# Performance work log

Hardware: AMD Instinct MI355X
Metric: run time of the kernel (lower is better)

## Reference

```python
import jax, jax.numpy as jnp
import numpy as np

B, N, D, H, DH, E, BIAS_DIM = 8, 512, 512, 8, 64, 32768, 8

def setup_inputs() -> dict:
    key = jax.random.key(0)
    ks = jax.random.split(key, 10)
    states = jax.random.normal(ks[0], (B, N, D), jnp.float32)
    key_states = jax.random.normal(ks[1], (B, N, D), jnp.float32)
    # causal mask, broadcastable over heads: [B,1,N,N]
    masks = jnp.broadcast_to(jnp.tril(jnp.ones((N, N), jnp.float32)), (B, 1, N, N))
    edge_type = jax.random.randint(ks[2], (E, 1), 0, BIAS_DIM, jnp.int32)
    b_idx = jax.random.randint(ks[3], (E, 1), 0, B, jnp.int32)
    q_idx = jax.random.randint(ks[4], (E, 1), 0, N, jnp.int32)
    k_idx = jax.random.randint(ks[5], (E, 1), 0, N, jnp.int32)
    attention_bias = jnp.concatenate([edge_type, b_idx, q_idx, k_idx], axis=1)
    s = 0.05
    Wq = jax.random.normal(ks[6], (D, H, DH), jnp.float32) * s
    Wk = jax.random.normal(ks[7], (D, H, DH), jnp.float32) * s
    Wv = jax.random.normal(ks[8], (D, H, DH), jnp.float32) * s
    k2 = jax.random.split(ks[9], 3)
    Wo = jax.random.normal(k2[0], (H, DH, D), jnp.float32) * s
    bias_embs = jax.random.normal(k2[1], (BIAS_DIM, DH), jnp.float32) * s
    bias_scalar = jax.random.normal(k2[2], (DH, 1), jnp.float32) * s
    return {"states": states, "key_states": key_states, "masks": masks,
            "attention_bias": attention_bias, "Wq": Wq, "Wk": Wk, "Wv": Wv,
            "Wo": Wo, "bias_embs": bias_embs, "bias_scalar": bias_scalar}

def reference(states, key_states, masks, attention_bias, Wq, Wk, Wv, Wo, bias_embs, bias_scalar):
    q = jnp.einsum('btd,dha->btha', states, Wq)
    k = jnp.einsum('btd,dha->btha', key_states, Wk)
    v = jnp.einsum('btd,dha->btha', key_states, Wv)
    alpha = jnp.einsum('bkha,bqha->bhqk', k, q)  # [B,H,Q,K]
    # sparse edge bias: embed edge types, project to scalar, scatter into [B,Q,K]
    et = attention_bias[:, 0]
    bias_vals = (bias_embs[et] @ bias_scalar)[:, 0]  # [E]
    bq, bk = alpha.shape[2], alpha.shape[3]
    bias_mat = jnp.zeros((alpha.shape[0], bq, bk), alpha.dtype)
    bias_mat = bias_mat.at[attention_bias[:, 1], attention_bias[:, 2], attention_bias[:, 3]].add(bias_vals)
    summed_keys = jnp.sum(k, axis=-1)  # [B,K,H]
    alpha = alpha + jnp.einsum('bqk,bkh->bhqk', bias_mat, summed_keys)
    alpha = alpha * jax.lax.rsqrt(jnp.float32(DH))
    neg = jnp.finfo(jnp.float32).min
    alpha = alpha * masks + (1.0 - jnp.ceil(masks)) * neg
    alpha = jax.nn.softmax(alpha, axis=-1)
    alpha = alpha * masks
    context = jnp.einsum('bhqk,bkha->bqha', alpha, v)
    return jnp.einsum('btha,had->btd', context, Wo)
```

## Files before the change

### kernel.cpp

```cpp
#include <hip/hip_runtime.h>

typedef unsigned short u16;
typedef unsigned int u32;
typedef __bf16 bf16x8 __attribute__((ext_vector_type(8)));
typedef float f32x4 __attribute__((ext_vector_type(4)));
typedef u16 u16x8 __attribute__((ext_vector_type(8)));
typedef u16 u16x4 __attribute__((ext_vector_type(4)));


__device__ __forceinline__ u16 f2b(float f) {
  union { float f; u32 i; } v; v.f = f;
  u32 r = v.i + 0x7fffu + ((v.i >> 16) & 1u);
  return (u16)(r >> 16);
}

#define GLL16(gp, lp)                                                      \
  __builtin_amdgcn_global_load_lds(                                       \
      (const __attribute__((address_space(1))) u32*)(gp),                 \
      (__attribute__((address_space(3))) u32*)(lp), 16, 0, 0)

__device__ __forceinline__ void stage64(const u16* g, u16* l, int wave, int lane) {
  int rsub = lane >> 3;
  int gs = (((lane & 7) ^ rsub) << 3);
  #pragma unroll
  for (int c = 0; c < 2; c++) {
    int ch = wave * 2 + c;
    GLL16(g + (size_t)(ch * 8 + rsub) * 512 + gs, l + ch * 512);
  }
}
__device__ __forceinline__ void stage128(const u16* g, u16* l, int wave, int lane) {
  int rsub = lane >> 3;
  int gs = (((lane & 7) ^ rsub) << 3);
  #pragma unroll
  for (int c = 0; c < 4; c++) {
    int ch = wave * 4 + c;
    GLL16(g + (size_t)(ch * 8 + rsub) * 512 + gs, l + ch * 512);
  }
}
__device__ __forceinline__ int swz(int row, int g) {
  return row * 64 + ((g ^ (row & 7)) << 3);
}

__global__ __launch_bounds__(256) void prologue(
    const float* __restrict__ states, const float* __restrict__ key_states,
    const float* __restrict__ Wq, const float* __restrict__ Wk,
    const float* __restrict__ Wv, const float* __restrict__ Wo,
    u16* __restrict__ sb, u16* __restrict__ kbin, u16* __restrict__ wbase,
    float* __restrict__ bias_mat) {
  __shared__ u16 t[32][33];
  int bid = blockIdx.x;
  int tid = threadIdx.x;
  if (bid < 2048) {
    const float* src = (bid >= 1024) ? key_states : states;
    u16* dst = (bid >= 1024) ? kbin : sb;
    int gid = (bid & 1023) * 256 + tid;
    const float4* sp = (const float4*)src + (size_t)gid * 2;
    float4 x0 = sp[0], x1 = sp[1];
    u16x8 p;
    p[0] = f2b(x0.x); p[1] = f2b(x0.y); p[2] = f2b(x0.z); p[3] = f2b(x0.w);
    p[4] = f2b(x1.x); p[5] = f2b(x1.y); p[6] = f2b(x1.z); p[7] = f2b(x1.w);
    *(u16x8*)(dst + (size_t)gid * 8) = p;
  } else if (bid < 3072) {
    int tt = bid - 2048;
    int z = tt >> 8, rem = tt & 255;
    int bx = rem & 15, by = rem >> 4;
    const float* src; float sc = 1.f;
    if (z == 0)      { src = Wq; sc = 0.125f; }
    else if (z == 1) { src = Wk; }
    else if (z == 2) { src = Wv; }
    else             { src = Wo; }
    u16* dst = wbase + (size_t)z * 262144;
    int tx = tid & 31, ty = tid >> 5;
    int c0 = bx * 32, r0 = by * 32;
    #pragma unroll
    for (int i = ty; i < 32; i += 8) t[i][tx] = f2b(src[(r0 + i) * 512 + c0 + tx] * sc);
    __syncthreads();
    #pragma unroll
    for (int i = ty; i < 32; i += 8) dst[(c0 + i) * 512 + r0 + tx] = t[tx][i];
  } else {
    int i = (bid - 3072) * 256 + tid;
    float4 z4 = {0.f, 0.f, 0.f, 0.f};
    ((float4*)bias_mat)[i] = z4;
  }
}

__global__ __launch_bounds__(256) void qkv_gemm(const u16* __restrict__ sb,
                                                const u16* __restrict__ kbin,
                                                const u16* __restrict__ wT,
                                                const int* __restrict__ ab,
                                                const float* __restrict__ be,
                                                const float* __restrict__ bsc,
                                                float* __restrict__ bias_m,
                                                u16* __restrict__ qb,
                                                u16* __restrict__ kbo,
                                                u16* __restrict__ vtb,
                                                float* __restrict__ summed,
                                                int n_edges) {
  __shared__ alignas(16) u16 As[2][64 * 64];
  __shared__ alignas(16) u16 Bs[2][128 * 64];
  __shared__ float ssum[4][64];
  __shared__ float tvs[8];
  int tid = threadIdx.x;
  int lane = tid & 63, wave = tid >> 6;
  int quad = lane >> 4, ln = lane & 15;
  int fb = blockIdx.y * 64 + blockIdx.x;

  if (tid < 8) {
    const float4* bev = (const float4*)(be + tid * 64);
    const float4* bscv = (const float4*)bsc;
    float s = 0.f;
    #pragma unroll
    for (int a4 = 0; a4 < 16; a4++) {
      float4 x = bev[a4], y = bscv[a4];
      s += x.x * y.x + x.y * y.y + x.z * y.z + x.w * y.w;
    }
    tvs[tid] = s * 0.125f;
  }
  __syncthreads();
  for (int e = fb * 256 + tid; e < n_edges; e += 768 * 256) {
    int et = ab[e * 4 + 0];
    int b  = ab[e * 4 + 1];
    int qi = ab[e * 4 + 2];
    int ki = ab[e * 4 + 3];
    atomicAdd(&bias_m[((size_t)b * 512 + qi) * 512 + ki], tvs[et]);
  }

  int row0 = blockIdx.x * 64;
  int col0 = blockIdx.y * 128;
  const u16* A = (col0 < 512) ? sb : kbin;
  const u16* Ab = A + (size_t)row0 * 512;
  const u16* Bb = wT + (size_t)col0 * 512;

  f32x4 acc[4][2];
  #pragma unroll
  for (int i = 0; i < 4; i++)
    #pragma unroll
    for (int j = 0; j < 2; j++) acc[i][j] = (f32x4){0.f, 0.f, 0.f, 0.f};

  stage64(Ab, As[0], wave, lane);
  stage128(Bb, Bs[0], wave, lane);

  int cur = 0;
  for (int k0 = 0; k0 < 512; k0 += 64) {
    __syncthreads();
    if (k0 < 448) {
      stage64(Ab + k0 + 64, As[cur ^ 1], wave, lane);
      stage128(Bb + k0 + 64, Bs[cur ^ 1], wave, lane);
    }
    #pragma unroll
    for (int s = 0; s < 2; s++) {
      bf16x8 af[4], bfv[2];
      #pragma unroll
      for (int i = 0; i < 4; i++)
        af[i] = *(bf16x8*)&As[cur][swz(i * 16 + ln, s * 4 + quad)];
      #pragma unroll
      for (int j = 0; j < 2; j++)
        bfv[j] = *(bf16x8*)&Bs[cur][swz(wave * 32 + j * 16 + ln, s * 4 + quad)];
      #pragma unroll
      for (int i = 0; i < 4; i++)
        #pragma unroll
        for (int j = 0; j < 2; j++)
          acc[i][j] = __builtin_amdgcn_mfma_f32_16x16x32_bf16(af[i], bfv[j], acc[i][j], 0, 0, 0);
    }
    cur ^= 1;
  }

  int region = col0 >> 9;
  int nbase = col0 & 511;
  if (region <= 1) {
    u16* Cout = region ? kbo : qb;
    #pragma unroll
    for (int i = 0; i < 4; i++)
      #pragma unroll
      for (int j = 0; j < 2; j++) {
        int mb = row0 + i * 16 + quad * 4;
        int n = nbase + wave * 32 + j * 16 + ln;
        #pragma unroll
        for (int r = 0; r < 4; r++)
          Cout[(size_t)(mb + r) * 512 + n] = f2b(acc[i][j][r]);
      }
    if (region == 1) {
      #pragma unroll
      for (int i = 0; i < 4; i++)
        #pragma unroll
        for (int r = 0; r < 4; r++) {
          float v = acc[i][0][r] + acc[i][1][r];
          v += __shfl_xor(v, 1);
          v += __shfl_xor(v, 2);
          v += __shfl_xor(v, 4);
          v += __shfl_xor(v, 8);
          if (ln == 0) ssum[wave][i * 16 + quad * 4 + r] = v;
        }
      __syncthreads();
      if (tid < 128) {
        int hl = tid >> 6, row = tid & 63;
        float s = ssum[hl * 2][row] + ssum[hl * 2 + 1][row];
        int m = row0 + row;
        int b = m >> 9, t = m & 511;
        int h = (nbase >> 6) + hl;
        summed[((size_t)(b * 8 + h)) * 512 + t] = s;
      }
    }
  } else {
    #pragma unroll
    for (int i = 0; i < 4; i++)
      #pragma unroll
      for (int j = 0; j < 2; j++) {
        int mb = row0 + i * 16 + quad * 4;
        int bb = mb >> 9, t0 = mb & 511;
        int a_abs = nbase + wave * 32 + j * 16 + ln;
        int h = a_abs >> 6, a = a_abs & 63;
        u16x4 p;
        p[0] = f2b(acc[i][j][0]); p[1] = f2b(acc[i][j][1]);
        p[2] = f2b(acc[i][j][2]); p[3] = f2b(acc[i][j][3]);
        *(u16x4*)&vtb[(((size_t)bb * 8 + h) * 64 + a) * 512 + t0] = p;
      }
  }
}

__global__ __launch_bounds__(256) void attn_mfma(const u16* __restrict__ q,
                                                 const u16* __restrict__ k,
                                                 const u16* __restrict__ vt,
                                                 const float* __restrict__ bias_mat,
                                                 const float* __restrict__ summed,
                                                 u16* __restrict__ ctx,
                                                 float* __restrict__ Opart,
                                                 float* __restrict__ ml) {
  __shared__ alignas(16) u16 Qs[64 * 64];
  __shared__ alignas(16) u16 Ks[2][64 * 64];
  __shared__ alignas(16) u16 Vs[2][64 * 64];
  __shared__ alignas(16) u16 Ps[4][16 * 72];
  int tid = threadIdx.x;
  int wave = tid >> 6, lane = tid & 63;
  int quad = lane >> 4, ln = lane & 15;
  int p2 = blockIdx.x;
  int bh, u;
  {
    const int fours[6] = {3, 4, 6, 8, 10, 11};
    const int threes[2] = {2, 9};
    const int ones[2] = {0, 5};
    const int twos[2] = {1, 7};
    if (p2 < 384)      { bh = p2 & 63; u = fours[p2 >> 6]; }
    else if (p2 < 512) { int q2 = p2 - 384; bh = q2 & 63; u = threes[q2 >> 6]; }
    else if (p2 < 640) { int q2 = p2 - 512; bh = q2 & 63; u = ones[q2 >> 6]; }
    else               { int q2 = p2 - 640; bh = q2 & 63; u = twos[q2 >> 6]; }
  }
  int b = bh >> 3, h = bh & 7;
  int qt, kb0, kbe, part = 0;
  bool partial;
  if (u < 4) { qt = u; kb0 = 0; kbe = u; partial = false; }
  else {
    int v = u - 4; qt = 4 + (v >> 1); part = v & 1; partial = true;
    if (part == 0) { kb0 = 0; kbe = 3; } else { kb0 = 4; kbe = qt; }
  }
  int q0 = qt * 64;

  const u16* qb_ = q + ((size_t)(b * 512 + q0)) * 512 + h * 64;
  const u16* kb_ = k + ((size_t)(b * 512)) * 512 + h * 64;
  const u16* vb_ = vt + ((size_t)bh * 64) * 512;

  stage64(qb_, Qs, wave, lane);
  stage64(kb_ + (size_t)kb0 * 64 * 512, Ks[0], wave, lane);
  stage64(vb_ + kb0 * 64, Vs[0], wave, lane);

  float m_r[4], l_r[4];
  f32x4 o[4];
  #pragma unroll
  for (int r = 0; r < 4; r++) { m_r[r] = -3.40282347e38f; l_r[r] = 0.f; }
  #pragma unroll
  for (int nt = 0; nt < 4; nt++) o[nt] = (f32x4){0.f, 0.f, 0.f, 0.f};

  int qrow = q0 + wave * 16 + quad * 4;

  float c_skv[4], c_bias[4][4];
  #pragma unroll
  for (int nt = 0; nt < 4; nt++) {
    int t = kb0 * 64 + nt * 16 + ln;
    c_skv[nt] = summed[bh * 512 + t];
    const float* bp2 = bias_mat + ((size_t)(b * 512 + qrow)) * 512 + t;
    #pragma unroll
    for (int r = 0; r < 4; r++) c_bias[nt][r] = bp2[(size_t)r * 512];
  }

  int cur = 0;
  for (int kb = kb0; kb <= kbe; kb++) {
    __syncthreads();

    float n_skv[4], n_bias[4][4];
    if (kb < kbe) {
      stage64(kb_ + (size_t)(kb + 1) * 64 * 512, Ks[cur ^ 1], wave, lane);
      stage64(vb_ + (kb + 1) * 64, Vs[cur ^ 1], wave, lane);
      #pragma unroll
      for (int nt = 0; nt < 4; nt++) {
        int t = (kb + 1) * 64 + nt * 16 + ln;
        n_skv[nt] = summed[bh * 512 + t];
        const float* bp2 = bias_mat + ((size_t)(b * 512 + qrow)) * 512 + t;
        #pragma unroll
        for (int r = 0; r < 4; r++) n_bias[nt][r] = bp2[(size_t)r * 512];
      }
    }

    bf16x8 aq0 = *(bf16x8*)&Qs[swz(wave * 16 + ln, quad)];
    bf16x8 aq1 = *(bf16x8*)&Qs[swz(wave * 16 + ln, 4 + quad)];
    f32x4 s[4];
    #pragma unroll
    for (int nt = 0; nt < 4; nt++) {
      bf16x8 b0 = *(bf16x8*)&Ks[cur][swz(nt * 16 + ln, quad)];
      bf16x8 b1 = *(bf16x8*)&Ks[cur][swz(nt * 16 + ln, 4 + quad)];
      s[nt] = (f32x4){0.f, 0.f, 0.f, 0.f};
      s[nt] = __builtin_amdgcn_mfma_f32_16x16x32_bf16(aq0, b0, s[nt], 0, 0, 0);
      s[nt] = __builtin_amdgcn_mfma_f32_16x16x32_bf16(aq1, b1, s[nt], 0, 0, 0);
    }

    #pragma unroll
    for (int nt = 0; nt < 4; nt++) {
      int t = kb * 64 + nt * 16 + ln;
      #pragma unroll
      for (int r = 0; r < 4; r++) {
        float val = s[nt][r] + c_bias[nt][r] * c_skv[nt];
        s[nt][r] = (t <= qrow + r) ? val : -3.40282347e38f;
      }
    }

    float alpha[4];
    #pragma unroll
    for (int r = 0; r < 4; r++) {
      float tm = fmaxf(fmaxf(s[0][r], s[1][r]), fmaxf(s[2][r], s[3][r]));
      #pragma unroll
      for (int off = 8; off; off >>= 1) tm = fmaxf(tm, __shfl_xor(tm, off));
      float mn = fmaxf(m_r[r], tm);
      alpha[r] = __expf(m_r[r] - mn);
      m_r[r] = mn;
      float rs = 0.f;
      #pragma unroll
      for (int nt = 0; nt < 4; nt++) {
        float pp = __expf(s[nt][r] - mn);
        s[nt][r] = pp;
        rs += pp;
      }
      #pragma unroll
      for (int off = 8; off; off >>= 1) rs += __shfl_xor(rs, off);
      l_r[r] = l_r[r] * alpha[r] + rs;
    }

    #pragma unroll
    for (int nt = 0; nt < 4; nt++)
      #pragma unroll
      for (int r = 0; r < 4; r++)
        Ps[wave][(quad * 4 + r) * 72 + nt * 16 + ln] = f2b(s[nt][r]);
    #pragma unroll
    for (int nt = 0; nt < 4; nt++)
      #pragma unroll
      for (int r = 0; r < 4; r++)
        o[nt][r] *= alpha[r];

    bf16x8 ap0 = *(bf16x8*)&Ps[wave][ln * 72 + quad * 8];
    bf16x8 ap1 = *(bf16x8*)&Ps[wave][ln * 72 + 32 + quad * 8];
    #pragma unroll
    for (int nt = 0; nt < 4; nt++) {
      bf16x8 b0 = *(bf16x8*)&Vs[cur][swz(nt * 16 + ln, quad)];
      bf16x8 b1 = *(bf16x8*)&Vs[cur][swz(nt * 16 + ln, 4 + quad)];
      o[nt] = __builtin_amdgcn_mfma_f32_16x16x32_bf16(ap0, b0, o[nt], 0, 0, 0);
      o[nt] = __builtin_amdgcn_mfma_f32_16x16x32_bf16(ap1, b1, o[nt], 0, 0, 0);
    }

    if (kb < kbe) {
      #pragma unroll
      for (int nt = 0; nt < 4; nt++) {
        c_skv[nt] = n_skv[nt];
        #pragma unroll
        for (int r = 0; r < 4; r++) c_bias[nt][r] = n_bias[nt][r];
      }
    }
    cur ^= 1;
  }

  if (!partial) {
    #pragma unroll
    for (int r = 0; r < 4; r++) {
      float inv = 1.f / l_r[r];
      int qr2 = qrow + r;
      u16* dst = ctx + ((size_t)(b * 512 + qr2)) * 512 + h * 64;
      #pragma unroll
      for (int nt = 0; nt < 4; nt++)
        dst[nt * 16 + ln] = f2b(o[nt][r] * inv);
    }
  } else {
    #pragma unroll
    for (int r = 0; r < 4; r++) {
      int row = qrow + r - 256;
      float* dst = Opart + (((size_t)(part * 64 + bh)) * 256 + row) * 64;
      #pragma unroll
      for (int nt = 0; nt < 4; nt++)
        dst[nt * 16 + ln] = o[nt][r];
    }
    if (ln == 0) {
      #pragma unroll
      for (int r = 0; r < 4; r++) {
        int row = qrow + r - 256;
        float* mp = ml + (((size_t)(part * 64 + bh)) * 256 + row) * 2;
        mp[0] = m_r[r];
        mp[1] = l_r[r];
      }
    }
  }
}

__device__ __forceinline__ void merge_stage(const float* __restrict__ Opart,
                                            const float* __restrict__ mlbuf,
                                            int row0, int k0, u16* dst, int tid) {
  int gi = tid * 2;
  int r = gi >> 3, g = gi & 7;
  int trow = (row0 & 511) - 256 + r;
  int b = row0 >> 9;
  int h = k0 >> 6;
  size_t i0 = ((size_t)(b * 8 + h)) * 256 + trow;
  size_t i1 = i0 + 64 * 256;
  float m0 = mlbuf[i0 * 2], l0 = mlbuf[i0 * 2 + 1];
  float m1 = mlbuf[i1 * 2], l1 = mlbuf[i1 * 2 + 1];
  float m = fmaxf(m0, m1);
  float a0 = __expf(m0 - m), a1 = __expf(m1 - m);
  float linv = 1.f / (l0 * a0 + l1 * a1);
  a0 *= linv; a1 *= linv;
  const float4* p0 = (const float4*)(Opart + i0 * 64 + g * 8);
  const float4* p1 = (const float4*)(Opart + i1 * 64 + g * 8);
  u16x8 q0, q1;
  #pragma unroll
  for (int c = 0; c < 2; c++) {
    float4 x0 = p0[c], x1 = p1[c];
    q0[c * 4 + 0] = f2b(x0.x * a0 + x1.x * a1);
    q0[c * 4 + 1] = f2b(x0.y * a0 + x1.y * a1);
    q0[c * 4 + 2] = f2b(x0.z * a0 + x1.z * a1);
    q0[c * 4 + 3] = f2b(x0.w * a0 + x1.w * a1);
  }
  #pragma unroll
  for (int c = 2; c < 4; c++) {
    float4 x0 = p0[c], x1 = p1[c];
    q1[(c - 2) * 4 + 0] = f2b(x0.x * a0 + x1.x * a1);
    q1[(c - 2) * 4 + 1] = f2b(x0.y * a0 + x1.y * a1);
    q1[(c - 2) * 4 + 2] = f2b(x0.z * a0 + x1.z * a1);
    q1[(c - 2) * 4 + 3] = f2b(x0.w * a0 + x1.w * a1);
  }
  *(u16x8*)&dst[swz(r, g)] = q0;
  *(u16x8*)&dst[swz(r, g + 1)] = q1;
}

__global__ __launch_bounds__(256) void out_gemm(const u16* __restrict__ A,
                                                const u16* __restrict__ BT,
                                                const float* __restrict__ Opart,
                                                const float* __restrict__ mlbuf,
                                                float* __restrict__ C) {
  __shared__ alignas(16) u16 As[2][64 * 64];
  __shared__ alignas(16) u16 Bs[2][64 * 64];
  int tid = threadIdx.x;
  int lane = tid & 63, wave = tid >> 6;
  int quad = lane >> 4, ln = lane & 15;
  int wr = wave >> 1, wc = wave & 1;
  int row0 = blockIdx.x * 64;
  int col0 = blockIdx.y * 64;
  bool mergeA = (row0 & 511) >= 256;
  const u16* Ab = A + (size_t)row0 * 512;
  const u16* Bb = BT + (size_t)col0 * 512;

  f32x4 acc[2][2];
  #pragma unroll
  for (int i = 0; i < 2; i++)
    #pragma unroll
    for (int j = 0; j < 2; j++) acc[i][j] = (f32x4){0.f, 0.f, 0.f, 0.f};

  if (mergeA) merge_stage(Opart, mlbuf, row0, 0, As[0], tid);
  else        stage64(Ab, As[0], wave, lane);
  stage64(Bb, Bs[0], wave, lane);

  int cur = 0;
  for (int k0 = 0; k0 < 512; k0 += 64) {
    __syncthreads();
    if (k0 < 448) {
      if (mergeA) merge_stage(Opart, mlbuf, row0, k0 + 64, As[cur ^ 1], tid);
      else        stage64(Ab + k0 + 64, As[cur ^ 1], wave, lane);
      stage64(Bb + k0 + 64, Bs[cur ^ 1], wave, lane);
    }
    #pragma unroll
    for (int s = 0; s < 2; s++) {
      bf16x8 af[2], bfv[2];
      #pragma unroll
      for (int i = 0; i < 2; i++)
        af[i] = *(bf16x8*)&As[cur][swz(wr * 32 + i * 16 + ln, s * 4 + quad)];
      #pragma unroll
      for (int j = 0; j < 2; j++)
        bfv[j] = *(bf16x8*)&Bs[cur][swz(wc * 32 + j * 16 + ln, s * 4 + quad)];
      #pragma unroll
      for (int i = 0; i < 2; i++)
        #pragma unroll
        for (int j = 0; j < 2; j++)
          acc[i][j] = __builtin_amdgcn_mfma_f32_16x16x32_bf16(af[i], bfv[j], acc[i][j], 0, 0, 0);
    }
    cur ^= 1;
  }
  #pragma unroll
  for (int i = 0; i < 2; i++)
    #pragma unroll
    for (int j = 0; j < 2; j++) {
      int mb = row0 + wr * 32 + i * 16 + quad * 4;
      int n = col0 + wc * 32 + j * 16 + ln;
      #pragma unroll
      for (int r = 0; r < 4; r++)
        C[(size_t)(mb + r) * 512 + n] = acc[i][j][r];
    }
}

extern "C" void kernel_launch(void* const* d_in, const int* in_sizes, int n_in,
                              void* d_out, int out_size, void* d_ws, size_t ws_size,
                              hipStream_t stream) {
  const float* states     = (const float*)d_in[0];
  const float* key_states = (const float*)d_in[1];
  const int*   ab         = (const int*)d_in[3];
  const float* Wq         = (const float*)d_in[4];
  const float* Wk         = (const float*)d_in[5];
  const float* Wv         = (const float*)d_in[6];
  const float* Wo         = (const float*)d_in[7];
  const float* be         = (const float*)d_in[8];
  const float* bsc        = (const float*)d_in[9];
  float* out = (float*)d_out;

  char* ws = (char*)d_ws;
  const size_t MB = 1024 * 1024;
  u16* wbase    = (u16*)(ws);
  u16* wot      = (u16*)(ws + 1536 * 1024);
  u16* sb       = (u16*)(ws + 2 * MB);
  u16* kbin     = (u16*)(ws + 6 * MB);
  u16* qb       = (u16*)(ws + 10 * MB);
  u16* kbo      = (u16*)(ws + 14 * MB);
  u16* vtb      = (u16*)(ws + 18 * MB);
  u16* ctxb     = (u16*)(ws + 22 * MB);
  float* bias_m = (float*)(ws + 26 * MB);
  float* summed = (float*)(ws + 34 * MB);
  float* Opart  = (float*)(ws + 35 * MB);
  float* mlbuf  = (float*)(ws + 43 * MB);

  int n_edges = in_sizes[3] / 4;

  prologue<<<dim3(5120), 256, 0, stream>>>(
      states, key_states, Wq, Wk, Wv, Wo, sb, kbin, wbase, bias_m);
  qkv_gemm<<<dim3(64, 12), 256, 0, stream>>>(
      sb, kbin, wbase, ab, be, bsc, bias_m, qb, kbo, vtb, summed, n_edges);
  attn_mfma<<<dim3(768), 256, 0, stream>>>(qb, kbo, vtb, bias_m, summed, ctxb, Opart, mlbuf);
  out_gemm<<<dim3(64, 8), 256, 0, stream>>>(ctxb, wot, Opart, mlbuf, out);
}
```

Before: 133.5 us.

## Fuse fp32-to-bf16 conversion and weight transpose into GEMM staging loops

Removes the prologue kernel that converted activations and weights to bf16 and transposed the weights into workspace. The qkv and output GEMMs now load fp32 data into registers, convert and transpose while writing to LDS, and prefetch the next tile in registers. The bias matrix is zeroed with hipMemsetAsync instead. This saves a kernel launch and a round trip of the converted data through memory. In exchange it adds an extra barrier per k-step, converts the weights redundantly in every block, and uses strided scalar weight loads in place of async global-to-LDS copies.

```diff
diff --git a/kernel.cpp b/kernel.cpp
--- a/kernel.cpp
+++ b/kernel.cpp
@@ -28,65 +28,15 @@
     GLL16(g + (size_t)(ch * 8 + rsub) * 512 + gs, l + ch * 512);
   }
 }
-__device__ __forceinline__ void stage128(const u16* g, u16* l, int wave, int lane) {
-  int rsub = lane >> 3;
-  int gs = (((lane & 7) ^ rsub) << 3);
-  #pragma unroll
-  for (int c = 0; c < 4; c++) {
-    int ch = wave * 4 + c;
-    GLL16(g + (size_t)(ch * 8 + rsub) * 512 + gs, l + ch * 512);
-  }
-}
 __device__ __forceinline__ int swz(int row, int g) {
   return row * 64 + ((g ^ (row & 7)) << 3);
 }
 
-__global__ __launch_bounds__(256) void prologue(
-    const float* __restrict__ states, const float* __restrict__ key_states,
-    const float* __restrict__ Wq, const float* __restrict__ Wk,
-    const float* __restrict__ Wv, const float* __restrict__ Wo,
-    u16* __restrict__ sb, u16* __restrict__ kbin, u16* __restrict__ wbase,
-    float* __restrict__ bias_mat) {
-  __shared__ u16 t[32][33];
-  int bid = blockIdx.x;
-  int tid = threadIdx.x;
-  if (bid < 2048) {
-    const float* src = (bid >= 1024) ? key_states : states;
-    u16* dst = (bid >= 1024) ? kbin : sb;
-    int gid = (bid & 1023) * 256 + tid;
-    const float4* sp = (const float4*)src + (size_t)gid * 2;
-    float4 x0 = sp[0], x1 = sp[1];
-    u16x8 p;
-    p[0] = f2b(x0.x); p[1] = f2b(x0.y); p[2] = f2b(x0.z); p[3] = f2b(x0.w);
-    p[4] = f2b(x1.x); p[5] = f2b(x1.y); p[6] = f2b(x1.z); p[7] = f2b(x1.w);
-    *(u16x8*)(dst + (size_t)gid * 8) = p;
-  } else if (bid < 3072) {
-    int tt = bid - 2048;
-    int z = tt >> 8, rem = tt & 255;
-    int bx = rem & 15, by = rem >> 4;
-    const float* src; float sc = 1.f;
-    if (z == 0)      { src = Wq; sc = 0.125f; }
-    else if (z == 1) { src = Wk; }
-    else if (z == 2) { src = Wv; }
-    else             { src = Wo; }
-    u16* dst = wbase + (size_t)z * 262144;
-    int tx = tid & 31, ty = tid >> 5;
-    int c0 = bx * 32, r0 = by * 32;
-    #pragma unroll
-    for (int i = ty; i < 32; i += 8) t[i][tx] = f2b(src[(r0 + i) * 512 + c0 + tx] * sc);
-    __syncthreads();
-    #pragma unroll
-    for (int i = ty; i < 32; i += 8) dst[(c0 + i) * 512 + r0 + tx] = t[tx][i];
-  } else {
-    int i = (bid - 3072) * 256 + tid;
-    float4 z4 = {0.f, 0.f, 0.f, 0.f};
-    ((float4*)bias_mat)[i] = z4;
-  }
-}
-
-__global__ __launch_bounds__(256) void qkv_gemm(const u16* __restrict__ sb,
-                                                const u16* __restrict__ kbin,
-                                                const u16* __restrict__ wT,
+__global__ __launch_bounds__(256) void qkv_gemm(const float* __restrict__ states,
+                                                const float* __restrict__ key_states,
+                                                const float* __restrict__ Wq,
+                                                const float* __restrict__ Wk,
+                                                const float* __restrict__ Wv,
                                                 const int* __restrict__ ab,
                                                 const float* __restrict__ be,
                                                 const float* __restrict__ bsc,
@@ -127,9 +77,16 @@
 
   int row0 = blockIdx.x * 64;
   int col0 = blockIdx.y * 128;
-  const u16* A = (col0 < 512) ? sb : kbin;
-  const u16* Ab = A + (size_t)row0 * 512;
-  const u16* Bb = wT + (size_t)col0 * 512;
+  int region = col0 >> 9;
+  int co = col0 & 511;
+  const float* A = (region == 0) ? states : key_states;
+  const float* Wz = (region == 0) ? Wq : (region == 1 ? Wk : Wv);
+  float sc = (region == 0) ? 0.125f : 1.f;
+
+  int ar = tid >> 2, aj = tid & 3;
+  const float* apA = A + (size_t)(row0 + ar) * 512 + aj * 16;
+  int bc = tid & 127, bh = tid >> 7;
+  const float* apB = Wz + (size_t)bh * 32 * 512 + co + bc;
 
   f32x4 acc[4][2];
   #pragma unroll
@@ -137,15 +94,41 @@
     #pragma unroll
     for (int j = 0; j < 2; j++) acc[i][j] = (f32x4){0.f, 0.f, 0.f, 0.f};
 
-  stage64(Ab, As[0], wave, lane);
-  stage128(Bb, Bs[0], wave, lane);
+  float4 rA[4];
+  float rB[32];
+  {
+    const float4* p = (const float4*)apA;
+    rA[0] = p[0]; rA[1] = p[1]; rA[2] = p[2]; rA[3] = p[3];
+    #pragma unroll
+    for (int i = 0; i < 32; i++) rB[i] = apB[(size_t)i * 512];
+  }
 
   int cur = 0;
   for (int k0 = 0; k0 < 512; k0 += 64) {
     __syncthreads();
+    {
+      u16x8 q0, q1;
+      q0[0]=f2b(rA[0].x); q0[1]=f2b(rA[0].y); q0[2]=f2b(rA[0].z); q0[3]=f2b(rA[0].w);
+      q0[4]=f2b(rA[1].x); q0[5]=f2b(rA[1].y); q0[6]=f2b(rA[1].z); q0[7]=f2b(rA[1].w);
+      q1[0]=f2b(rA[2].x); q1[1]=f2b(rA[2].y); q1[2]=f2b(rA[2].z); q1[3]=f2b(rA[2].w);
+      q1[4]=f2b(rA[3].x); q1[5]=f2b(rA[3].y); q1[6]=f2b(rA[3].z); q1[7]=f2b(rA[3].w);
+      *(u16x8*)&As[cur][swz(ar, 2 * aj)]     = q0;
+      *(u16x8*)&As[cur][swz(ar, 2 * aj + 1)] = q1;
+    }
+    #pragma unroll
+    for (int g2 = 0; g2 < 4; g2++) {
+      u16x8 pk;
+      #pragma unroll
+      for (int e8 = 0; e8 < 8; e8++) pk[e8] = f2b(rB[g2 * 8 + e8] * sc);
+      *(u16x8*)&Bs[cur][swz(bc, bh * 4 + g2)] = pk;
+    }
+    __syncthreads();
     if (k0 < 448) {
-      stage64(Ab + k0 + 64, As[cur ^ 1], wave, lane);
-      stage128(Bb + k0 + 64, Bs[cur ^ 1], wave, lane);
+      const float4* p = (const float4*)(apA + k0 + 64);
+      rA[0] = p[0]; rA[1] = p[1]; rA[2] = p[2]; rA[3] = p[3];
+      const float* bp = apB + (size_t)(k0 + 64) * 512;
+      #pragma unroll
+      for (int i = 0; i < 32; i++) rB[i] = bp[(size_t)i * 512];
     }
     #pragma unroll
     for (int s = 0; s < 2; s++) {
@@ -165,8 +148,7 @@
     cur ^= 1;
   }
 
-  int region = col0 >> 9;
-  int nbase = col0 & 511;
+  int nbase = co;
   if (region <= 1) {
     u16* Cout = region ? kbo : qb;
     #pragma unroll
@@ -446,7 +428,7 @@
 }
 
 __global__ __launch_bounds__(256) void out_gemm(const u16* __restrict__ A,
-                                                const u16* __restrict__ BT,
+                                                const float* __restrict__ Wo,
                                                 const float* __restrict__ Opart,
                                                 const float* __restrict__ mlbuf,
                                                 float* __restrict__ C) {
@@ -460,7 +442,8 @@
   int col0 = blockIdx.y * 64;
   bool mergeA = (row0 & 511) >= 256;
   const u16* Ab = A + (size_t)row0 * 512;
-  const u16* Bb = BT + (size_t)col0 * 512;
+  int bc2 = tid & 63, bq = tid >> 6;
+  const float* apB = Wo + (size_t)bq * 16 * 512 + col0 + bc2;
 
   f32x4 acc[2][2];
   #pragma unroll
@@ -468,17 +451,28 @@
     #pragma unroll
     for (int j = 0; j < 2; j++) acc[i][j] = (f32x4){0.f, 0.f, 0.f, 0.f};
 
-  if (mergeA) merge_stage(Opart, mlbuf, row0, 0, As[0], tid);
-  else        stage64(Ab, As[0], wave, lane);
-  stage64(Bb, Bs[0], wave, lane);
+  float rB[16];
+  #pragma unroll
+  for (int i = 0; i < 16; i++) rB[i] = apB[(size_t)i * 512];
+  if (!mergeA) stage64(Ab, As[0], wave, lane);
 
   int cur = 0;
   for (int k0 = 0; k0 < 512; k0 += 64) {
     __syncthreads();
+    #pragma unroll
+    for (int g2 = 0; g2 < 2; g2++) {
+      u16x8 pk;
+      #pragma unroll
+      for (int e8 = 0; e8 < 8; e8++) pk[e8] = f2b(rB[g2 * 8 + e8]);
+      *(u16x8*)&Bs[cur][swz(bc2, bq * 2 + g2)] = pk;
+    }
+    if (mergeA) merge_stage(Opart, mlbuf, row0, k0, As[cur], tid);
+    __syncthreads();
     if (k0 < 448) {
-      if (mergeA) merge_stage(Opart, mlbuf, row0, k0 + 64, As[cur ^ 1], tid);
-      else        stage64(Ab + k0 + 64, As[cur ^ 1], wave, lane);
-      stage64(Bb + k0 + 64, Bs[cur ^ 1], wave, lane);
+      const float* bp = apB + (size_t)(k0 + 64) * 512;
+      #pragma unroll
+      for (int i = 0; i < 16; i++) rB[i] = bp[(size_t)i * 512];
+      if (!mergeA) stage64(Ab + k0 + 64, As[cur ^ 1], wave, lane);
     }
     #pragma unroll
     for (int s = 0; s < 2; s++) {
@@ -525,25 +519,21 @@
 
   char* ws = (char*)d_ws;
   const size_t MB = 1024 * 1024;
-  u16* wbase    = (u16*)(ws);
-  u16* wot      = (u16*)(ws + 1536 * 1024);
-  u16* sb       = (u16*)(ws + 2 * MB);
-  u16* kbin     = (u16*)(ws + 6 * MB);
-  u16* qb       = (u16*)(ws + 10 * MB);
-  u16* kbo      = (u16*)(ws + 14 * MB);
-  u16* vtb      = (u16*)(ws + 18 * MB);
-  u16* ctxb     = (u16*)(ws + 22 * MB);
-  float* bias_m = (float*)(ws + 26 * MB);
-  float* summed = (float*)(ws + 34 * MB);
-  float* Opart  = (float*)(ws + 35 * MB);
-  float* mlbuf  = (float*)(ws + 43 * MB);
+  u16* qb       = (u16*)(ws);
+  u16* kbo      = (u16*)(ws + 4 * MB);
+  u16* vtb      = (u16*)(ws + 8 * MB);
+  u16* ctxb     = (u16*)(ws + 12 * MB);
+  float* bias_m = (float*)(ws + 16 * MB);
+  float* summed = (float*)(ws + 24 * MB);
+  float* Opart  = (float*)(ws + 25 * MB);
+  float* mlbuf  = (float*)(ws + 33 * MB);
 
   int n_edges = in_sizes[3] / 4;
 
-  prologue<<<dim3(5120), 256, 0, stream>>>(
-      states, key_states, Wq, Wk, Wv, Wo, sb, kbin, wbase, bias_m);
+  hipMemsetAsync(bias_m, 0, (size_t)8 * MB, stream);
   qkv_gemm<<<dim3(64, 12), 256, 0, stream>>>(
-      sb, kbin, wbase, ab, be, bsc, bias_m, qb, kbo, vtb, summed, n_edges);
+      states, key_states, Wq, Wk, Wv, ab, be, bsc, bias_m,
+      qb, kbo, vtb, summed, n_edges);
   attn_mfma<<<dim3(768), 256, 0, stream>>>(qb, kbo, vtb, bias_m, summed, ctxb, Opart, mlbuf);
-  out_gemm<<<dim3(64, 8), 256, 0, stream>>>(ctxb, wot, Opart, mlbuf, out);
-}
+  out_gemm<<<dim3(64, 8), 256, 0, stream>>>(ctxb, Wo, Opart, mlbuf, out);
+}
```

New measurement: 139.1 us. 4.2% more time.

## Drop split-K attention partials and merge; schedule longest query tiles first

Applied to the files above, without the earlier changes.

Removes the split-KV scheme where late query tiles were processed in two partial blocks whose results were merged inside the output GEMM. Each of the 512 attention blocks now handles one full query tile, and the longest (last) tiles are launched first to balance load. Bias scatter atomics are skipped for edges above the causal diagonal, since those entries are masked out anyway. The context buffer reuses the states buffer. This trades the extra partial writes and merge work for less parallelism and a longer tail on the largest tiles.

```diff
diff --git a/kernel.cpp b/kernel.cpp
--- a/kernel.cpp
+++ b/kernel.cpp
@@ -122,7 +122,8 @@
     int b  = ab[e * 4 + 1];
     int qi = ab[e * 4 + 2];
     int ki = ab[e * 4 + 3];
-    atomicAdd(&bias_m[((size_t)b * 512 + qi) * 512 + ki], tvs[et]);
+    if (ki <= qi)
+      atomicAdd(&bias_m[((size_t)b * 512 + qi) * 512 + ki], tvs[et]);
   }
 
   int row0 = blockIdx.x * 64;
@@ -223,9 +224,7 @@
                                                  const u16* __restrict__ vt,
                                                  const float* __restrict__ bias_mat,
                                                  const float* __restrict__ summed,
-                                                 u16* __restrict__ ctx,
-                                                 float* __restrict__ Opart,
-                                                 float* __restrict__ ml) {
+                                                 u16* __restrict__ ctx) {
   __shared__ alignas(16) u16 Qs[64 * 64];
   __shared__ alignas(16) u16 Ks[2][64 * 64];
   __shared__ alignas(16) u16 Vs[2][64 * 64];
@@ -234,34 +233,20 @@
   int wave = tid >> 6, lane = tid & 63;
   int quad = lane >> 4, ln = lane & 15;
   int p2 = blockIdx.x;
-  int bh, u;
-  {
-    const int fours[6] = {3, 4, 6, 8, 10, 11};
-    const int threes[2] = {2, 9};
-    const int ones[2] = {0, 5};
-    const int twos[2] = {1, 7};
-    if (p2 < 384)      { bh = p2 & 63; u = fours[p2 >> 6]; }
-    else if (p2 < 512) { int q2 = p2 - 384; bh = q2 & 63; u = threes[q2 >> 6]; }
-    else if (p2 < 640) { int q2 = p2 - 512; bh = q2 & 63; u = ones[q2 >> 6]; }
-    else               { int q2 = p2 - 640; bh = q2 & 63; u = twos[q2 >> 6]; }
-  }
+  int bh, qt;
+  if (p2 < 256) { bh = p2 & 63; qt = 7 - (p2 >> 6); }
+  else          { int q2 = p2 - 256; bh = q2 & 63; qt = q2 >> 6; }
   int b = bh >> 3, h = bh & 7;
-  int qt, kb0, kbe, part = 0;
-  bool partial;
-  if (u < 4) { qt = u; kb0 = 0; kbe = u; partial = false; }
-  else {
-    int v = u - 4; qt = 4 + (v >> 1); part = v & 1; partial = true;
-    if (part == 0) { kb0 = 0; kbe = 3; } else { kb0 = 4; kbe = qt; }
-  }
   int q0 = qt * 64;
+  int kbe = qt;
 
   const u16* qb_ = q + ((size_t)(b * 512 + q0)) * 512 + h * 64;
   const u16* kb_ = k + ((size_t)(b * 512)) * 512 + h * 64;
   const u16* vb_ = vt + ((size_t)bh * 64) * 512;
 
   stage64(qb_, Qs, wave, lane);
-  stage64(kb_ + (size_t)kb0 * 64 * 512, Ks[0], wave, lane);
-  stage64(vb_ + kb0 * 64, Vs[0], wave, lane);
+  stage64(kb_, Ks[0], wave, lane);
+  stage64(vb_, Vs[0], wave, lane);
 
   float m_r[4], l_r[4];
   f32x4 o[4];
@@ -275,7 +260,7 @@
   float c_skv[4], c_bias[4][4];
   #pragma unroll
   for (int nt = 0; nt < 4; nt++) {
-    int t = kb0 * 64 + nt * 16 + ln;
+    int t = nt * 16 + ln;
     c_skv[nt] = summed[bh * 512 + t];
     const float* bp2 = bias_mat + ((size_t)(b * 512 + qrow)) * 512 + t;
     #pragma unroll
@@ -283,7 +268,7 @@
   }
 
   int cur = 0;
-  for (int kb = kb0; kb <= kbe; kb++) {
+  for (int kb = 0; kb <= kbe; kb++) {
     __syncthreads();
 
     float n_skv[4], n_bias[4][4];
@@ -375,80 +360,19 @@
     cur ^= 1;
   }
 
-  if (!partial) {
-    #pragma unroll
-    for (int r = 0; r < 4; r++) {
-      float inv = 1.f / l_r[r];
-      int qr2 = qrow + r;
-      u16* dst = ctx + ((size_t)(b * 512 + qr2)) * 512 + h * 64;
-      #pragma unroll
-      for (int nt = 0; nt < 4; nt++)
-        dst[nt * 16 + ln] = f2b(o[nt][r] * inv);
-    }
-  } else {
-    #pragma unroll
-    for (int r = 0; r < 4; r++) {
-      int row = qrow + r - 256;
-      float* dst = Opart + (((size_t)(part * 64 + bh)) * 256 + row) * 64;
-      #pragma unroll
-      for (int nt = 0; nt < 4; nt++)
-        dst[nt * 16 + ln] = o[nt][r];
-    }
-    if (ln == 0) {
-      #pragma unroll
-      for (int r = 0; r < 4; r++) {
-        int row = qrow + r - 256;
-        float* mp = ml + (((size_t)(part * 64 + bh)) * 256 + row) * 2;
-        mp[0] = m_r[r];
-        mp[1] = l_r[r];
-      }
-    }
-  }
-}
-
-__device__ __forceinline__ void merge_stage(const float* __restrict__ Opart,
-                                            const float* __restrict__ mlbuf,
-                                            int row0, int k0, u16* dst, int tid) {
-  int gi = tid * 2;
-  int r = gi >> 3, g = gi & 7;
-  int trow = (row0 & 511) - 256 + r;
-  int b = row0 >> 9;
-  int h = k0 >> 6;
-  size_t i0 = ((size_t)(b * 8 + h)) * 256 + trow;
-  size_t i1 = i0 + 64 * 256;
-  float m0 = mlbuf[i0 * 2], l0 = mlbuf[i0 * 2 + 1];
-  float m1 = mlbuf[i1 * 2], l1 = mlbuf[i1 * 2 + 1];
-  float m = fmaxf(m0, m1);
-  float a0 = __expf(m0 - m), a1 = __expf(m1 - m);
-  float linv = 1.f / (l0 * a0 + l1 * a1);
-  a0 *= linv; a1 *= linv;
-  const float4* p0 = (const float4*)(Opart + i0 * 64 + g * 8);
-  const float4* p1 = (const float4*)(Opart + i1 * 64 + g * 8);
-  u16x8 q0, q1;
-  #pragma unroll
-  for (int c = 0; c < 2; c++) {
-    float4 x0 = p0[c], x1 = p1[c];
-    q0[c * 4 + 0] = f2b(x0.x * a0 + x1.x * a1);
-    q0[c * 4 + 1] = f2b(x0.y * a0 + x1.y * a1);
-    q0[c * 4 + 2] = f2b(x0.z * a0 + x1.z * a1);
-    q0[c * 4 + 3] = f2b(x0.w * a0 + x1.w * a1);
-  }
-  #pragma unroll
-  for (int c = 2; c < 4; c++) {
-    float4 x0 = p0[c], x1 = p1[c];
-    q1[(c - 2) * 4 + 0] = f2b(x0.x * a0 + x1.x * a1);
-    q1[(c - 2) * 4 + 1] = f2b(x0.y * a0 + x1.y * a1);
-    q1[(c - 2) * 4 + 2] = f2b(x0.z * a0 + x1.z * a1);
-    q1[(c - 2) * 4 + 3] = f2b(x0.w * a0 + x1.w * a1);
-  }
-  *(u16x8*)&dst[swz(r, g)] = q0;
-  *(u16x8*)&dst[swz(r, g + 1)] = q1;
+  #pragma unroll
+  for (int r = 0; r < 4; r++) {
+    float inv = 1.f / l_r[r];
+    int qr2 = qrow + r;
+    u16* dst = ctx + ((size_t)(b * 512 + qr2)) * 512 + h * 64;
+    #pragma unroll
+    for (int nt = 0; nt < 4; nt++)
+      dst[nt * 16 + ln] = f2b(o[nt][r] * inv);
+  }
 }
 
 __global__ __launch_bounds__(256) void out_gemm(const u16* __restrict__ A,
                                                 const u16* __restrict__ BT,
-                                                const float* __restrict__ Opart,
-                                                const float* __restrict__ mlbuf,
                                                 float* __restrict__ C) {
   __shared__ alignas(16) u16 As[2][64 * 64];
   __shared__ alignas(16) u16 Bs[2][64 * 64];
@@ -458,7 +382,6 @@
   int wr = wave >> 1, wc = wave & 1;
   int row0 = blockIdx.x * 64;
   int col0 = blockIdx.y * 64;
-  bool mergeA = (row0 & 511) >= 256;
   const u16* Ab = A + (size_t)row0 * 512;
   const u16* Bb = BT + (size_t)col0 * 512;
 
@@ -468,16 +391,14 @@
     #pragma unroll
     for (int j = 0; j < 2; j++) acc[i][j] = (f32x4){0.f, 0.f, 0.f, 0.f};
 
-  if (mergeA) merge_stage(Opart, mlbuf, row0, 0, As[0], tid);
-  else        stage64(Ab, As[0], wave, lane);
+  stage64(Ab, As[0], wave, lane);
   stage64(Bb, Bs[0], wave, lane);
 
   int cur = 0;
   for (int k0 = 0; k0 < 512; k0 += 64) {
     __syncthreads();
     if (k0 < 448) {
-      if (mergeA) merge_stage(Opart, mlbuf, row0, k0 + 64, As[cur ^ 1], tid);
-      else        stage64(Ab + k0 + 64, As[cur ^ 1], wave, lane);
+      stage64(Ab + k0 + 64, As[cur ^ 1], wave, lane);
       stage64(Bb + k0 + 64, Bs[cur ^ 1], wave, lane);
     }
     #pragma unroll
@@ -528,15 +449,13 @@
   u16* wbase    = (u16*)(ws);
   u16* wot      = (u16*)(ws + 1536 * 1024);
   u16* sb       = (u16*)(ws + 2 * MB);
+  u16* ctxb     = sb;
   u16* kbin     = (u16*)(ws + 6 * MB);
   u16* qb       = (u16*)(ws + 10 * MB);
   u16* kbo      = (u16*)(ws + 14 * MB);
   u16* vtb      = (u16*)(ws + 18 * MB);
-  u16* ctxb     = (u16*)(ws + 22 * MB);
-  float* bias_m = (float*)(ws + 26 * MB);
-  float* summed = (float*)(ws + 34 * MB);
-  float* Opart  = (float*)(ws + 35 * MB);
-  float* mlbuf  = (float*)(ws + 43 * MB);
+  float* bias_m = (float*)(ws + 22 * MB);
+  float* summed = (float*)(ws + 30 * MB);
 
   int n_edges = in_sizes[3] / 4;
 
@@ -544,6 +463,6 @@
       states, key_states, Wq, Wk, Wv, Wo, sb, kbin, wbase, bias_m);
   qkv_gemm<<<dim3(64, 12), 256, 0, stream>>>(
       sb, kbin, wbase, ab, be, bsc, bias_m, qb, kbo, vtb, summed, n_edges);
-  attn_mfma<<<dim3(768), 256, 0, stream>>>(qb, kbo, vtb, bias_m, summed, ctxb, Opart, mlbuf);
-  out_gemm<<<dim3(64, 8), 256, 0, stream>>>(ctxb, wot, Opart, mlbuf, out);
-}
+  attn_mfma<<<dim3(512), 256, 0, stream>>>(qb, kbo, vtb, bias_m, summed, ctxb);
+  out_gemm<<<dim3(64, 8), 256, 0, stream>>>(ctxb, wot, out);
+}
```

After: 131.4 us (median of 2 runs). About the same (-1.6%).
